# Optimization experiments

Hardware: AMD Instinct MI355X
Metric: run time of the kernel (lower is better)

The kernel has to match this reference:

```python
import jax, jax.numpy as jnp
import numpy as np
import math

B, S, D = 2, 2048, 2048
HQ, HKV = 16, 4            # query heads, kv heads
HD = D // HQ               # head dim = 128
REPS = HQ // HKV           # queries per kv head = 4
KVD = HKV * HD             # 512


def setup_inputs() -> dict:
    key = jax.random.key(0)
    ks = jax.random.split(key, 7)
    s = 0.02
    return {
        "hidden_states": jax.random.normal(ks[0], (B, S, D), dtype=jnp.float32),
        "Wq": jax.random.normal(ks[1], (D, D), dtype=jnp.float32) * s,
        "bq": jnp.zeros((D,), dtype=jnp.float32),
        "Wk": jax.random.normal(ks[2], (D, KVD), dtype=jnp.float32) * s,
        "bk": jnp.zeros((KVD,), dtype=jnp.float32),
        "Wv": jax.random.normal(ks[3], (D, KVD), dtype=jnp.float32) * s,
        "bv": jnp.zeros((KVD,), dtype=jnp.float32),
    }


def reference(hidden_states, Wq, bq, Wk, bk, Wv, bv):
    b, s, d = hidden_states.shape
    # Projections
    q = hidden_states @ Wq + bq                      # [B,S,D]
    k = hidden_states @ Wk + bk                      # [B,S,KVD]
    v = hidden_states @ Wv + bv                      # [B,S,KVD]
    # Split heads. torch repeat_kv_heads uses .repeat (tile), so expanded
    # head h maps to kv head (h mod HKV). Reshape q heads as (REPS, HKV)
    # so axis g indexes the kv head, matching that tiling exactly.
    q = q.reshape(b, s, HQ, HD).transpose(0, 2, 1, 3)          # [B,HQ,S,hd]
    q = q.reshape(b, REPS, HKV, s, HD)                          # [B,R,G,S,hd]
    k = k.reshape(b, s, HKV, HD).transpose(0, 2, 1, 3)          # [B,G,S,hd]
    v = v.reshape(b, s, HKV, HD).transpose(0, 2, 1, 3)          # [B,G,S,hd]
    scale = 1.0 / math.sqrt(HD)
    scores = jnp.einsum('brgsd,bgtd->brgst', q, k) * scale      # [B,R,G,S,S]
    probs = jax.nn.softmax(scores, axis=-1)
    ctx = jnp.einsum('brgst,bgtd->brgsd', probs, v)             # [B,R,G,S,hd]
    ctx = ctx.reshape(b, HQ, s, HD).transpose(0, 2, 1, 3)       # [B,S,HQ,hd]
    return ctx.reshape(b, s, HQ * HD)                            # [B,S,D]
```

## Files before the change

kernel.cpp:

```cpp
#include <hip/hip_runtime.h>
#include <hip/hip_bf16.h>

#define QSCALE   0.08838834764831845f
#define QKSCALE  0.1275174468755322f

typedef __attribute__((ext_vector_type(8))) short bh8;
typedef __attribute__((ext_vector_type(4))) float fx4;
typedef __attribute__((ext_vector_type(4))) short sh4;

typedef const __attribute__((address_space(1))) unsigned GAu;
typedef __attribute__((address_space(3))) unsigned LAu;

__device__ __forceinline__ short f2bf(float f) {
    unsigned u = __float_as_uint(f);
    unsigned r = u + 0x7fffu + ((u >> 16) & 1u);
    return (short)(r >> 16);
}

__device__ __forceinline__ unsigned pk_bf16(float x, float y) {
    union { __hip_bfloat162 h; unsigned u; } cv;
    cv.h = __float22bfloat162_rn(float2{x, y});
    return cv.u;
}

__global__ __launch_bounds__(256) void cvt_x(const float* __restrict__ x,
                                             short* __restrict__ o) {
    int i = blockIdx.x * 256 + threadIdx.x;
    float4 v = ((const float4*)x)[i];
    sh4 s;
    s.x = f2bf(v.x); s.y = f2bf(v.y); s.z = f2bf(v.z); s.w = f2bf(v.w);
    ((sh4*)o)[i] = s;
}

__global__ __launch_bounds__(256) void transpose_w(const float* __restrict__ w,
                                                   short* __restrict__ wt,
                                                   int K, int N) {
    __shared__ float tile[32][33];
    int nb = blockIdx.x, kb = blockIdx.y;
    int tx = threadIdx.x & 31, ty = threadIdx.x >> 5;
#pragma unroll
    for (int j = 0; j < 4; ++j) {
        int k = kb * 32 + ty + j * 8;
        tile[ty + j * 8][tx] = w[(size_t)k * N + nb * 32 + tx];
    }
    __syncthreads();
#pragma unroll
    for (int j = 0; j < 4; ++j) {
        int n = nb * 32 + ty + j * 8;
        wt[(size_t)n * K + kb * 32 + tx] = f2bf(tile[tx][ty + j * 8]);
    }
}

__global__ __launch_bounds__(256) void proj_gemm(
    const short* __restrict__ X,
    const short* __restrict__ WqT,
    const short* __restrict__ WkT,
    const short* __restrict__ WvT,
    const float* __restrict__ bq, const float* __restrict__ bk,
    const float* __restrict__ bv,
    short* __restrict__ Qb, short* __restrict__ Kpk, short* __restrict__ Vpk) {
    __shared__ short As0[128 * 32];
    __shared__ short As1[128 * 32];
    __shared__ short Bs0[128 * 32];
    __shared__ short Bs1[128 * 32];

    const int tid = threadIdx.x;
    const int bm = blockIdx.x;
    const int ntg = blockIdx.y;

    const short* Wm; const float* bias; int col0, kind;
    if (ntg < 16)      { Wm = WqT; bias = bq; col0 = ntg * 128;        kind = 0; }
    else if (ntg < 20) { Wm = WkT; bias = bk; col0 = (ntg - 16) * 128; kind = 1; }
    else               { Wm = WvT; bias = bv; col0 = (ntg - 20) * 128; kind = 2; }

    const int w = tid >> 6, lane = tid & 63, quad = lane >> 4, l16 = lane & 15;

    fx4 acc[2][8];
#pragma unroll
    for (int i = 0; i < 2; ++i)
#pragma unroll
        for (int j = 0; j < 8; ++j) acc[i][j] = fx4{0.f, 0.f, 0.f, 0.f};

    const int srow = w * 16 + (lane >> 2);
    const int scol = (((lane & 3) ^ ((lane >> 2) & 3)) * 8);
    const short* Ag = X + (size_t)(bm * 128 + srow) * 2048 + scol;
    const short* Bg = Wm + (size_t)(col0 + srow) * 2048 + scol;
    const int stoff = w * 512;

    const int fchunk = (quad ^ (l16 & 3)) * 8;
    const int aoff0 = (w * 32 + l16) * 32 + fchunk;
    const int aoff1 = aoff0 + 512;
    const int boff  = l16 * 32 + fchunk;

    const short* pA00 = As0 + aoff0;  const short* pA01 = As0 + aoff1;
    const short* pA10 = As1 + aoff0;  const short* pA11 = As1 + aoff1;
    const short* pB0  = Bs0 + boff;   const short* pB1  = Bs1 + boff;

#define PG_STAGE(AsD, BsD, ktile)                                               \
    do {                                                                        \
        const int k0_ = (ktile) * 32;                                           \
        _Pragma("unroll")                                                       \
        for (int j = 0; j < 2; ++j) {                                           \
            __builtin_amdgcn_global_load_lds(                                   \
                (GAu*)(Ag + (size_t)(j * 64) * 2048 + k0_),                     \
                (LAu*)(AsD + stoff + j * 2048), 16, 0, 0);                      \
            __builtin_amdgcn_global_load_lds(                                   \
                (GAu*)(Bg + (size_t)(j * 64) * 2048 + k0_),                     \
                (LAu*)(BsD + stoff + j * 2048), 16, 0, 0);                      \
        }                                                                       \
    } while (0)

#define PG_COMPUTE(pA0_, pA1_, pB_)                                             \
    do {                                                                        \
        bh8 af0 = *(const bh8*)(pA0_);                                          \
        bh8 af1 = *(const bh8*)(pA1_);                                          \
        _Pragma("unroll")                                                       \
        for (int nt = 0; nt < 8; ++nt) {                                        \
            bh8 bf = *(const bh8*)((pB_) + nt * 512);                           \
            acc[0][nt] = __builtin_amdgcn_mfma_f32_16x16x32_bf16(af0, bf, acc[0][nt], 0, 0, 0); \
            acc[1][nt] = __builtin_amdgcn_mfma_f32_16x16x32_bf16(af1, bf, acc[1][nt], 0, 0, 0); \
        }                                                                       \
    } while (0)

    PG_STAGE(As0, Bs0, 0);
    __syncthreads();

    for (int kt = 0; kt < 64; kt += 2) {
        PG_STAGE(As1, Bs1, kt + 1);
        PG_COMPUTE(pA00, pA01, pB0);
        __syncthreads();

        if (kt < 62) PG_STAGE(As0, Bs0, kt + 2);
        PG_COMPUTE(pA10, pA11, pB1);
        __syncthreads();
    }
#undef PG_STAGE
#undef PG_COMPUTE

#pragma unroll
    for (int mt = 0; mt < 2; ++mt) {
        int srow2 = bm * 128 + w * 32 + mt * 16 + quad * 4;
#pragma unroll
        for (int nt = 0; nt < 8; ++nt) {
            int c = col0 + nt * 16 + l16;
            float bval = bias[c];
#pragma unroll
            for (int r = 0; r < 4; ++r) {
                int sg = srow2 + r;
                int b = sg >> 11, s = sg & 2047;
                float v = acc[mt][nt][r] + bval;
                int hd = c & 127;
                if (kind == 0) {
                    v *= QKSCALE;
                    int h = c >> 7;
                    Qb[(((size_t)(b * 16 + h) * 2048 + s) << 7) + hd] = f2bf(v);
                } else if (kind == 1) {
                    int g = c >> 7;
                    int ktt = s >> 6, tl = s & 63;
                    int fnt = tl >> 4, fl16 = tl & 15;
                    int ks = hd >> 5, qd = (hd >> 3) & 3, j = hd & 7;
                    size_t frag = (((size_t)(b * 4 + g) * 32 + ktt) * 16 + fnt * 4 + ks);
                    Kpk[frag * 512 + (qd * 16 + fl16) * 8 + j] = f2bf(v);
                } else {
                    int g = c >> 7;
                    int ktt = s >> 6, tl = s & 63;
                    int ts = tl >> 5, qd = (tl >> 3) & 3, j = tl & 7;
                    int fnt = hd >> 4, fl16 = hd & 15;
                    size_t frag = (((size_t)(b * 4 + g) * 32 + ktt) * 16 + fnt * 2 + ts);
                    Vpk[frag * 512 + (qd * 16 + fl16) * 8 + j] = f2bf(v);
                }
            }
        }
    }
}

__global__ __launch_bounds__(128, 2) void attn(
    const short* __restrict__ Qb,
    const short* __restrict__ Kpk,
    const short* __restrict__ Vpk,
    float* __restrict__ out) {
    __shared__ short Ks0[8 * 512];
    __shared__ short Ks1[8 * 512];
    __shared__ short Vs0[8 * 512];
    __shared__ short Vs1[8 * 512];
    __shared__ __align__(16) unsigned Ps[2][32][20];

    const int bid = blockIdx.x;
    const int gb = bid & 7;
    const int rep = (bid >> 3) & 3;
    const int qt = bid >> 5;
    const int b = gb >> 2, g = gb & 3;
    const int h = rep * 4 + g;
    const int tid = threadIdx.x, w = tid >> 6, lane = tid & 63;
    const int quad = lane >> 4, l16 = lane & 15;

    bh8 qf[2][4];
#pragma unroll
    for (int rg = 0; rg < 2; ++rg) {
        int s = qt * 64 + w * 32 + rg * 16 + l16;
        const short* qp = Qb + (((size_t)(b * 16 + h) * 2048 + s) << 7);
#pragma unroll
        for (int ks = 0; ks < 4; ++ks)
            qf[rg][ks] = *(const bh8*)(qp + ks * 32 + quad * 8);
    }

    const short* kbase = Kpk + ((size_t)gb * 32) * 8192;
    const short* vbase = Vpk + ((size_t)gb * 32) * 8192;

    const short* pK0 = Ks0 + lane * 8;
    const short* pK1 = Ks1 + lane * 8;
    const short* pV0 = Vs0 + lane * 8;
    const short* pV1 = Vs1 + lane * 8;

    fx4 ctx[2][8];
#pragma unroll
    for (int rg = 0; rg < 2; ++rg)
#pragma unroll
        for (int j = 0; j < 8; ++j) ctx[rg][j] = fx4{0.f, 0.f, 0.f, 0.f};
    float l_part[2][4] = {{0.f, 0.f, 0.f, 0.f}, {0.f, 0.f, 0.f, 0.f}};

#define AT_STAGE(KsD, VsD, kn)                                                  \
    do {                                                                        \
        const short* kp_ = kbase + (size_t)(kn) * 4096;                         \
        const short* vp_ = vbase + (size_t)((kn) >> 1) * 8192 + ((kn) & 1) * 512;\
        _Pragma("unroll")                                                       \
        for (int i = 0; i < 4; ++i) {                                           \
            int f = w * 4 + i;                                                  \
            __builtin_amdgcn_global_load_lds((GAu*)(kp_ + f * 512 + lane * 8),  \
                                             (LAu*)(KsD + f * 512), 16, 0, 0);  \
            __builtin_amdgcn_global_load_lds((GAu*)(vp_ + (size_t)f * 1024 + lane * 8),\
                                             (LAu*)(VsD + f * 512), 16, 0, 0);  \
        }                                                                       \
    } while (0)

#define AT_COMPUTE(pKC, pVC)                                                    \
    do {                                                                        \
        fx4 sc[2][2];                                                           \
        sc[0][0] = fx4{0.f, 0.f, 0.f, 0.f}; sc[0][1] = fx4{0.f, 0.f, 0.f, 0.f}; \
        sc[1][0] = fx4{0.f, 0.f, 0.f, 0.f}; sc[1][1] = fx4{0.f, 0.f, 0.f, 0.f}; \
        _Pragma("unroll")                                                       \
        for (int nti = 0; nti < 2; ++nti) {                                     \
            _Pragma("unroll")                                                   \
            for (int ks = 0; ks < 4; ++ks) {                                    \
                bh8 kf = *(const bh8*)((pKC) + (nti * 4 + ks) * 512);           \
                sc[0][nti] = __builtin_amdgcn_mfma_f32_16x16x32_bf16(qf[0][ks], kf, sc[0][nti], 0, 0, 0); \
                sc[1][nti] = __builtin_amdgcn_mfma_f32_16x16x32_bf16(qf[1][ks], kf, sc[1][nti], 0, 0, 0); \
            }                                                                   \
        }                                                                       \
        _Pragma("unroll")                                                       \
        for (int rg = 0; rg < 2; ++rg) {                                        \
            _Pragma("unroll")                                                   \
            for (int r = 0; r < 4; ++r) {                                       \
                float p0 = __builtin_amdgcn_exp2f(sc[rg][0][r]);                \
                float p1 = __builtin_amdgcn_exp2f(sc[rg][1][r]);                \
                l_part[rg][r] += p0 + p1;                                       \
                Ps[w][rg * 16 + quad * 4 + r][l16] = pk_bf16(p0, p1);           \
            }                                                                   \
        }                                                                       \
        bh8 pa[2];                                                              \
        _Pragma("unroll")                                                       \
        for (int rg = 0; rg < 2; ++rg) {                                        \
            const unsigned* prow = &Ps[w][rg * 16 + l16][(quad & 1) * 8];       \
            uint4 lo = *(const uint4*)(prow);                                   \
            uint4 hi = *(const uint4*)(prow + 4);                               \
            unsigned dw[8] = {lo.x, lo.y, lo.z, lo.w, hi.x, hi.y, hi.z, hi.w};  \
            unsigned sel = (quad & 2) ? 0x07060302u : 0x05040100u;              \
            unsigned a[4];                                                      \
            _Pragma("unroll")                                                   \
            for (int j = 0; j < 4; ++j)                                         \
                a[j] = __builtin_amdgcn_perm(dw[2 * j + 1], dw[2 * j], sel);    \
            pa[rg] = *(const bh8*)a;                                            \
        }                                                                       \
        _Pragma("unroll")                                                       \
        for (int nt = 0; nt < 8; ++nt) {                                        \
            bh8 vf = *(const bh8*)((pVC) + nt * 512);                           \
            ctx[0][nt] = __builtin_amdgcn_mfma_f32_16x16x32_bf16(pa[0], vf, ctx[0][nt], 0, 0, 0); \
            ctx[1][nt] = __builtin_amdgcn_mfma_f32_16x16x32_bf16(pa[1], vf, ctx[1][nt], 0, 0, 0); \
        }                                                                       \
    } while (0)

    AT_STAGE(Ks0, Vs0, 0);
    __syncthreads();

    for (int kt = 0; kt < 64; kt += 2) {
        AT_STAGE(Ks1, Vs1, kt + 1);
        AT_COMPUTE(pK0, pV0);
        __syncthreads();

        if (kt < 62) AT_STAGE(Ks0, Vs0, kt + 2);
        AT_COMPUTE(pK1, pV1);
        __syncthreads();
    }
#undef AT_STAGE
#undef AT_COMPUTE

#pragma unroll
    for (int rg = 0; rg < 2; ++rg) {
        int srow = qt * 64 + w * 32 + rg * 16 + quad * 4;
#pragma unroll
        for (int r = 0; r < 4; ++r) {
            float lsum = l_part[rg][r];
            lsum += __shfl_xor(lsum, 1);
            lsum += __shfl_xor(lsum, 2);
            lsum += __shfl_xor(lsum, 4);
            lsum += __shfl_xor(lsum, 8);
            float inv = 1.f / lsum;
            size_t rowoff = ((size_t)b * 2048 + (srow + r)) * 2048 + h * 128;
#pragma unroll
            for (int nt = 0; nt < 8; ++nt)
                out[rowoff + nt * 16 + l16] = ctx[rg][nt][r] * inv;
        }
    }
}

extern "C" void kernel_launch(void* const* d_in, const int* in_sizes, int n_in,
                              void* d_out, int out_size, void* d_ws, size_t ws_size,
                              hipStream_t stream) {
    const float* hs = (const float*)d_in[0];
    const float* Wq = (const float*)d_in[1];
    const float* bq = (const float*)d_in[2];
    const float* Wk = (const float*)d_in[3];
    const float* bk = (const float*)d_in[4];
    const float* Wv = (const float*)d_in[5];
    const float* bv = (const float*)d_in[6];
    float* out = (float*)d_out;

    char* ws = (char*)d_ws;
    short* Xbf = (short*)(ws);
    short* WqT = (short*)(ws + 16777216);
    short* WkT = (short*)(ws + 25165824);
    short* WvT = (short*)(ws + 27262976);
    short* Qb  = (short*)(ws + 29360128);
    short* Kpk = (short*)(ws + 46137344);
    short* Vpk = (short*)(ws + 50331648);

    cvt_x<<<8192, 256, 0, stream>>>(hs, Xbf);
    transpose_w<<<dim3(64, 64), 256, 0, stream>>>(Wq, WqT, 2048, 2048);
    transpose_w<<<dim3(16, 64), 256, 0, stream>>>(Wk, WkT, 2048, 512);
    transpose_w<<<dim3(16, 64), 256, 0, stream>>>(Wv, WvT, 2048, 512);
    proj_gemm<<<dim3(32, 24), 256, 0, stream>>>(Xbf, WqT, WkT, WvT, bq, bk, bv,
                                                Qb, Kpk, Vpk);
    attn<<<1024, 128, 0, stream>>>(Qb, Kpk, Vpk, out);
}
```

Before: 267.1 us.

## Compute transposed scores so P feeds PV MFMA directly from registers

The K packing layout now permutes key positions within 32-key blocks, and the QK MFMA swaps its operands so the score accumulator holds S^T per lane. The exponentiated probabilities can then be packed straight into the A-operand fragment for the PV MFMA. This removes the per-tile LDS write/read round trip and the byte-permute shuffle for P. Row sums become one partial per lane, reduced across quads at the end and gathered with shuffles. It depends on the key permutation in the projection kernel matching the register layout of the MFMA output exactly.

```diff
diff --git a/kernel.cpp b/kernel.cpp
--- a/kernel.cpp
+++ b/kernel.cpp
@@ -156,10 +156,10 @@
                     Qb[(((size_t)(b * 16 + h) * 2048 + s) << 7) + hd] = f2bf(v);
                 } else if (kind == 1) {
                     int g = c >> 7;
-                    int ktt = s >> 6, tl = s & 63;
-                    int fnt = tl >> 4, fl16 = tl & 15;
+                    int kt32 = s >> 5, u = s & 31;
+                    int nti = (u >> 2) & 1, fl16 = (u >> 3) * 4 + (u & 3);
                     int ks = hd >> 5, qd = (hd >> 3) & 3, j = hd & 7;
-                    size_t frag = (((size_t)(b * 4 + g) * 32 + ktt) * 16 + fnt * 4 + ks);
+                    size_t frag = (((size_t)(b * 4 + g) * 64 + kt32) * 8 + nti * 4 + ks);
                     Kpk[frag * 512 + (qd * 16 + fl16) * 8 + j] = f2bf(v);
                 } else {
                     int g = c >> 7;
@@ -183,7 +183,6 @@
     __shared__ short Ks1[8 * 512];
     __shared__ short Vs0[8 * 512];
     __shared__ short Vs1[8 * 512];
-    __shared__ __align__(16) unsigned Ps[2][32][20];
 
     const int bid = blockIdx.x;
     const int gb = bid & 7;
@@ -217,7 +216,7 @@
     for (int rg = 0; rg < 2; ++rg)
 #pragma unroll
         for (int j = 0; j < 8; ++j) ctx[rg][j] = fx4{0.f, 0.f, 0.f, 0.f};
-    float l_part[2][4] = {{0.f, 0.f, 0.f, 0.f}, {0.f, 0.f, 0.f, 0.f}};
+    float l_part[2] = {0.f, 0.f};
 
 #define AT_STAGE(KsD, VsD, kn)                                                  \
     do {                                                                        \
@@ -243,32 +242,27 @@
             _Pragma("unroll")                                                   \
             for (int ks = 0; ks < 4; ++ks) {                                    \
                 bh8 kf = *(const bh8*)((pKC) + (nti * 4 + ks) * 512);           \
-                sc[0][nti] = __builtin_amdgcn_mfma_f32_16x16x32_bf16(qf[0][ks], kf, sc[0][nti], 0, 0, 0); \
-                sc[1][nti] = __builtin_amdgcn_mfma_f32_16x16x32_bf16(qf[1][ks], kf, sc[1][nti], 0, 0, 0); \
+                sc[0][nti] = __builtin_amdgcn_mfma_f32_16x16x32_bf16(kf, qf[0][ks], sc[0][nti], 0, 0, 0); \
+                sc[1][nti] = __builtin_amdgcn_mfma_f32_16x16x32_bf16(kf, qf[1][ks], sc[1][nti], 0, 0, 0); \
             }                                                                   \
         }                                                                       \
+        bh8 pa[2];                                                              \
         _Pragma("unroll")                                                       \
         for (int rg = 0; rg < 2; ++rg) {                                        \
-            _Pragma("unroll")                                                   \
-            for (int r = 0; r < 4; ++r) {                                       \
-                float p0 = __builtin_amdgcn_exp2f(sc[rg][0][r]);                \
-                float p1 = __builtin_amdgcn_exp2f(sc[rg][1][r]);                \
-                l_part[rg][r] += p0 + p1;                                       \
-                Ps[w][rg * 16 + quad * 4 + r][l16] = pk_bf16(p0, p1);           \
-            }                                                                   \
-        }                                                                       \
-        bh8 pa[2];                                                              \
-        _Pragma("unroll")                                                       \
-        for (int rg = 0; rg < 2; ++rg) {                                        \
-            const unsigned* prow = &Ps[w][rg * 16 + l16][(quad & 1) * 8];       \
-            uint4 lo = *(const uint4*)(prow);                                   \
-            uint4 hi = *(const uint4*)(prow + 4);                               \
-            unsigned dw[8] = {lo.x, lo.y, lo.z, lo.w, hi.x, hi.y, hi.z, hi.w};  \
-            unsigned sel = (quad & 2) ? 0x07060302u : 0x05040100u;              \
+            float e0 = __builtin_amdgcn_exp2f(sc[rg][0][0]);                    \
+            float e1 = __builtin_amdgcn_exp2f(sc[rg][0][1]);                    \
+            float e2 = __builtin_amdgcn_exp2f(sc[rg][0][2]);                    \
+            float e3 = __builtin_amdgcn_exp2f(sc[rg][0][3]);                    \
+            float e4 = __builtin_amdgcn_exp2f(sc[rg][1][0]);                    \
+            float e5 = __builtin_amdgcn_exp2f(sc[rg][1][1]);                    \
+            float e6 = __builtin_amdgcn_exp2f(sc[rg][1][2]);                    \
+            float e7 = __builtin_amdgcn_exp2f(sc[rg][1][3]);                    \
+            l_part[rg] += ((e0 + e1) + (e2 + e3)) + ((e4 + e5) + (e6 + e7));    \
             unsigned a[4];                                                      \
-            _Pragma("unroll")                                                   \
-            for (int j = 0; j < 4; ++j)                                         \
-                a[j] = __builtin_amdgcn_perm(dw[2 * j + 1], dw[2 * j], sel);    \
+            a[0] = pk_bf16(e0, e1);                                             \
+            a[1] = pk_bf16(e2, e3);                                             \
+            a[2] = pk_bf16(e4, e5);                                             \
+            a[3] = pk_bf16(e6, e7);                                             \
             pa[rg] = *(const bh8*)a;                                            \
         }                                                                       \
         _Pragma("unroll")                                                       \
@@ -296,15 +290,13 @@
 
 #pragma unroll
     for (int rg = 0; rg < 2; ++rg) {
+        float lsum = l_part[rg];
+        lsum += __shfl_xor(lsum, 16);
+        lsum += __shfl_xor(lsum, 32);
         int srow = qt * 64 + w * 32 + rg * 16 + quad * 4;
 #pragma unroll
         for (int r = 0; r < 4; ++r) {
-            float lsum = l_part[rg][r];
-            lsum += __shfl_xor(lsum, 1);
-            lsum += __shfl_xor(lsum, 2);
-            lsum += __shfl_xor(lsum, 4);
-            lsum += __shfl_xor(lsum, 8);
-            float inv = 1.f / lsum;
+            float inv = 1.f / __shfl(lsum, quad * 4 + r);
             size_t rowoff = ((size_t)b * 2048 + (srow + r)) * 2048 + h * 128;
 #pragma unroll
             for (int nt = 0; nt < 8; ++nt)
```

New measurement: 278.4 us. 4.2% more time.
